# Optimization experiments

Hardware: AMD Instinct MI355X
Metric: run time of the kernel (lower is better)

Reference implementation:

```python
import jax, jax.numpy as jnp
import numpy as np


def setup_inputs() -> dict:
    key = jax.random.key(0)
    x = jax.random.normal(key, (4, 4096, 128), dtype=jnp.float32)
    return {"x": x}


def reference(x) -> jnp.ndarray:
    # Unnormalized bilinear self-attention with Q=K=V=x (no softmax).
    # scores[b,t,s] = sum_d x[b,t,d] x[b,s,d]; out[b,t,d] = sum_s scores[b,t,s] x[b,s,d]
    scores = jnp.einsum('btd,bsd->bts', x, x)  # [B,T,T]
    out = jnp.einsum('bts,bsd->btd', scores, x)  # [B,T,D]
    return out
```

## Files before the change

### kernel.cpp

```cpp
#include <hip/hip_runtime.h>

#define BATCH 4
#define T 4096
#define D 128
#define CHUNKS 64
#define ROWS1 64
#define ROWS2 64
#define ST1 72
#define S2 136

typedef __attribute__((ext_vector_type(4))) float f32x4;
typedef __attribute__((ext_vector_type(8))) short bf16x8;

__device__ __forceinline__ unsigned short f2b(float f) {
    unsigned u = __builtin_bit_cast(unsigned, f);
    u += 0x7FFFu + ((u >> 16) & 1u);
    return (unsigned short)(u >> 16);
}
__device__ __forceinline__ float b2f(unsigned short h) {
    return __builtin_bit_cast(float, (unsigned)h << 16);
}

__global__ __launch_bounds__(256) void k_gram(const float* __restrict__ x,
                                              unsigned short* __restrict__ part) {
    __shared__ unsigned short XT[D * ST1];
    const int blk = blockIdx.x;
    const int b = blk >> 6, chunk = blk & 63;
    const float* xp = x + ((size_t)b * T + (size_t)chunk * ROWS1) * D;
    const int tid = threadIdx.x;

    #pragma unroll
    for (int pass = 0; pass < 8; pass++) {
        const int slot = (tid >> 6) + 4 * pass;
        const int dd = 2 * (tid & 7) + 16 * (slot & 7);
        const int tpg = ((tid >> 3) & 7) + 8 * (slot >> 3);
        const int t = 2 * tpg;
        float2 f0 = *(const float2*)(xp + (size_t)t * D + dd);
        float2 f1 = *(const float2*)(xp + (size_t)(t + 1) * D + dd);
        unsigned u0 = (unsigned)f2b(f0.x) | ((unsigned)f2b(f1.x) << 16);
        unsigned u1 = (unsigned)f2b(f0.y) | ((unsigned)f2b(f1.y) << 16);
        *(unsigned*)(XT + dd * ST1 + 2 * tpg) = u0;
        *(unsigned*)(XT + (dd + 1) * ST1 + 2 * tpg) = u1;
    }
    __syncthreads();

    const int lane = tid & 63, w = tid >> 6;
    const int m = lane & 15, q = lane >> 4;
    const int m0 = w * 32;

    f32x4 acc[2][8];
    #pragma unroll
    for (int mi = 0; mi < 2; mi++)
        #pragma unroll
        for (int ni = 0; ni < 8; ni++) acc[mi][ni] = (f32x4){0.f, 0.f, 0.f, 0.f};

    #pragma unroll
    for (int s = 0; s < 2; s++) {
        bf16x8 av[2], bv[8];
        #pragma unroll
        for (int mi = 0; mi < 2; mi++)
            av[mi] = *(const bf16x8*)(XT + (m0 + mi * 16 + m) * ST1 + q * 8 + s * 32);
        #pragma unroll
        for (int ni = 0; ni < 8; ni++)
            bv[ni] = *(const bf16x8*)(XT + (ni * 16 + m) * ST1 + q * 8 + s * 32);
        #pragma unroll
        for (int mi = 0; mi < 2; mi++)
            #pragma unroll
            for (int ni = 0; ni < 8; ni++)
                acc[mi][ni] = __builtin_amdgcn_mfma_f32_16x16x32_bf16(av[mi], bv[ni], acc[mi][ni], 0, 0, 0);
    }

    unsigned short* pp = part + (size_t)blk * (D * D);
    #pragma unroll
    for (int mi = 0; mi < 2; mi++)
        #pragma unroll
        for (int ni = 0; ni < 8; ni++) {
            const int row0 = m0 + mi * 16 + q * 4;
            const int col = ni * 16 + m;
            #pragma unroll
            for (int r = 0; r < 4; r++)
                pp[(size_t)(row0 + r) * D + col] = f2b(acc[mi][ni][r]);
        }
}

__global__ __launch_bounds__(256) void k_reduce_g(const unsigned short* __restrict__ part,
                                                  unsigned short* __restrict__ g) {
    const int o = blockIdx.x * 256 + threadIdx.x;
    const int b = o >> 14;
    const int e = o & 16383;
    const unsigned short* p = part + ((size_t)b * CHUNKS) * (D * D) + e;
    float s[8];
    #pragma unroll
    for (int i = 0; i < 8; i++) s[i] = 0.f;
    for (int c = 0; c < CHUNKS; c += 8) {
        #pragma unroll
        for (int i = 0; i < 8; i++)
            s[i] += b2f(p[(size_t)(c + i) * (D * D)]);
    }
    float sum = ((s[0] + s[1]) + (s[2] + s[3])) + ((s[4] + s[5]) + (s[6] + s[7]));
    g[o] = f2b(sum);
}

__global__ __launch_bounds__(256) void k_xg_mfma(const float* __restrict__ x,
                                                 const unsigned short* __restrict__ g,
                                                 float* __restrict__ out) {
    __shared__ unsigned short Xs[ROWS2 * S2];
    __shared__ unsigned short Gs[D * S2];
    const int blk = blockIdx.x;
    const int b = blk >> 6, chunk = blk & 63;
    const float* xp = x + ((size_t)b * T + (size_t)chunk * ROWS2) * D;
    const unsigned short* gp = g + (size_t)b * (D * D);
    const int tid = threadIdx.x;

    {
        const int dg = tid & 31, tr = tid >> 5;
        #pragma unroll
        for (int ii = 0; ii < 8; ii++) {
            const int t = tr + ii * 8;
            float4 v = ((const float4*)(xp + t * D))[dg];
            ushort4 pk;
            pk.x = f2b(v.x); pk.y = f2b(v.y); pk.z = f2b(v.z); pk.w = f2b(v.w);
            *(ushort4*)(Xs + t * S2 + dg * 4) = pk;
        }
    }
    {
        const int f4 = tid & 15, r = tid >> 4;
        #pragma unroll
        for (int ii = 0; ii < 8; ii++) {
            const int row = r + ii * 16;
            uint4 gv = ((const uint4*)(gp + row * D))[f4];
            *(uint4*)(Gs + row * S2 + f4 * 8) = gv;
        }
    }
    __syncthreads();

    const int lane = tid & 63, w = tid >> 6;
    const int m = lane & 15, q = lane >> 4;

    f32x4 acc[8];
    #pragma unroll
    for (int ni = 0; ni < 8; ni++) acc[ni] = (f32x4){0.f, 0.f, 0.f, 0.f};

    const unsigned short* arow = Xs + (w * 16 + m) * S2 + q * 8;
    const unsigned short* brow = Gs + m * S2 + q * 8;

    #pragma unroll
    for (int s = 0; s < 4; s++) {
        bf16x8 a = *(const bf16x8*)(arow + s * 32);
        #pragma unroll
        for (int ni = 0; ni < 8; ni++) {
            bf16x8 bb = *(const bf16x8*)(brow + ni * 16 * S2 + s * 32);
            acc[ni] = __builtin_amdgcn_mfma_f32_16x16x32_bf16(a, bb, acc[ni], 0, 0, 0);
        }
    }

    float* op = out + ((size_t)b * T + (size_t)chunk * ROWS2) * D;
    const int row0 = w * 16 + q * 4;
    #pragma unroll
    for (int ni = 0; ni < 8; ni++)
        #pragma unroll
        for (int r = 0; r < 4; r++)
            op[(row0 + r) * D + ni * 16 + m] = acc[ni][r];
}

extern "C" void kernel_launch(void* const* d_in, const int* in_sizes, int n_in,
                              void* d_out, int out_size, void* d_ws, size_t ws_size,
                              hipStream_t stream) {
    const float* x = (const float*)d_in[0];
    float* out = (float*)d_out;

    const size_t part_elems = (size_t)BATCH * CHUNKS * D * D;
    unsigned short* part = (unsigned short*)d_ws;
    unsigned short* g = part + part_elems;

    k_gram<<<BATCH * CHUNKS, 256, 0, stream>>>(x, part);
    k_reduce_g<<<BATCH * D * D / 256, 256, 0, stream>>>(part, g);
    k_xg_mfma<<<BATCH * 64, 256, 0, stream>>>(x, g, out);
}
```

Before: 69.44 us.

## Fuse gram, reduce, and XG kernels into one cooperative kernel with grid syncs

Merges the three launches (per-chunk gram partials, cross-chunk reduction, X·G product) into one cooperative kernel that uses two grid-wide syncs in place of kernel boundaries. The bf16 row-major copy of X is kept in shared memory from the first phase, so the third phase does not reload and reconvert x from global memory. This removes two launch gaps and one pass over x, at the cost of grid-sync overhead and a requirement that all 256 blocks be co-resident.

```diff
diff --git a/kernel.cpp b/kernel.cpp
--- a/kernel.cpp
+++ b/kernel.cpp
@@ -1,11 +1,13 @@
 #include <hip/hip_runtime.h>
+#include <hip/hip_cooperative_groups.h>
+
+namespace cg = cooperative_groups;
 
 #define BATCH 4
 #define T 4096
 #define D 128
 #define CHUNKS 64
-#define ROWS1 64
-#define ROWS2 64
+#define ROWS 64
 #define ST1 72
 #define S2 136
 
@@ -21,14 +23,21 @@
     return __builtin_bit_cast(float, (unsigned)h << 16);
 }
 
-__global__ __launch_bounds__(256) void k_gram(const float* __restrict__ x,
-                                              unsigned short* __restrict__ part) {
-    __shared__ unsigned short XT[D * ST1];
+__global__ __launch_bounds__(256) void k_fused(const float* __restrict__ x,
+                                               unsigned short* __restrict__ part,
+                                               unsigned short* __restrict__ g,
+                                               float* __restrict__ out) {
+    __shared__ unsigned short Xs[ROWS * S2];
+    __shared__ unsigned short XG[D * S2];
+
     const int blk = blockIdx.x;
     const int b = blk >> 6, chunk = blk & 63;
-    const float* xp = x + ((size_t)b * T + (size_t)chunk * ROWS1) * D;
+    const float* xp = x + ((size_t)b * T + (size_t)chunk * ROWS) * D;
     const int tid = threadIdx.x;
+    const int lane = tid & 63, w = tid >> 6;
+    const int m = lane & 15, q = lane >> 4;
 
+    unsigned short* XT = XG;
     #pragma unroll
     for (int pass = 0; pass < 8; pass++) {
         const int slot = (tid >> 6) + 4 * pass;
@@ -37,93 +46,78 @@
         const int t = 2 * tpg;
         float2 f0 = *(const float2*)(xp + (size_t)t * D + dd);
         float2 f1 = *(const float2*)(xp + (size_t)(t + 1) * D + dd);
-        unsigned u0 = (unsigned)f2b(f0.x) | ((unsigned)f2b(f1.x) << 16);
-        unsigned u1 = (unsigned)f2b(f0.y) | ((unsigned)f2b(f1.y) << 16);
-        *(unsigned*)(XT + dd * ST1 + 2 * tpg) = u0;
-        *(unsigned*)(XT + (dd + 1) * ST1 + 2 * tpg) = u1;
+        const unsigned short b00 = f2b(f0.x), b01 = f2b(f0.y);
+        const unsigned short b10 = f2b(f1.x), b11 = f2b(f1.y);
+        *(unsigned*)(XT + dd * ST1 + 2 * tpg)       = (unsigned)b00 | ((unsigned)b10 << 16);
+        *(unsigned*)(XT + (dd + 1) * ST1 + 2 * tpg) = (unsigned)b01 | ((unsigned)b11 << 16);
+        *(unsigned*)(Xs + (size_t)t * S2 + dd)       = (unsigned)b00 | ((unsigned)b01 << 16);
+        *(unsigned*)(Xs + (size_t)(t + 1) * S2 + dd) = (unsigned)b10 | ((unsigned)b11 << 16);
     }
     __syncthreads();
 
-    const int lane = tid & 63, w = tid >> 6;
-    const int m = lane & 15, q = lane >> 4;
-    const int m0 = w * 32;
-
-    f32x4 acc[2][8];
-    #pragma unroll
-    for (int mi = 0; mi < 2; mi++)
-        #pragma unroll
-        for (int ni = 0; ni < 8; ni++) acc[mi][ni] = (f32x4){0.f, 0.f, 0.f, 0.f};
-
-    #pragma unroll
-    for (int s = 0; s < 2; s++) {
-        bf16x8 av[2], bv[8];
-        #pragma unroll
-        for (int mi = 0; mi < 2; mi++)
-            av[mi] = *(const bf16x8*)(XT + (m0 + mi * 16 + m) * ST1 + q * 8 + s * 32);
-        #pragma unroll
-        for (int ni = 0; ni < 8; ni++)
-            bv[ni] = *(const bf16x8*)(XT + (ni * 16 + m) * ST1 + q * 8 + s * 32);
+    {
+        const int m0 = w * 32;
+        f32x4 acc[2][8];
         #pragma unroll
         for (int mi = 0; mi < 2; mi++)
             #pragma unroll
+            for (int ni = 0; ni < 8; ni++) acc[mi][ni] = (f32x4){0.f, 0.f, 0.f, 0.f};
+
+        #pragma unroll
+        for (int s = 0; s < 2; s++) {
+            bf16x8 av[2], bv[8];
+            #pragma unroll
+            for (int mi = 0; mi < 2; mi++)
+                av[mi] = *(const bf16x8*)(XT + (m0 + mi * 16 + m) * ST1 + q * 8 + s * 32);
+            #pragma unroll
             for (int ni = 0; ni < 8; ni++)
-                acc[mi][ni] = __builtin_amdgcn_mfma_f32_16x16x32_bf16(av[mi], bv[ni], acc[mi][ni], 0, 0, 0);
+                bv[ni] = *(const bf16x8*)(XT + (ni * 16 + m) * ST1 + q * 8 + s * 32);
+            #pragma unroll
+            for (int mi = 0; mi < 2; mi++)
+                #pragma unroll
+                for (int ni = 0; ni < 8; ni++)
+                    acc[mi][ni] = __builtin_amdgcn_mfma_f32_16x16x32_bf16(av[mi], bv[ni], acc[mi][ni], 0, 0, 0);
+        }
+
+        unsigned short* pp = part + (size_t)blk * (D * D);
+        #pragma unroll
+        for (int mi = 0; mi < 2; mi++)
+            #pragma unroll
+            for (int ni = 0; ni < 8; ni++) {
+                const int row0 = m0 + mi * 16 + q * 4;
+                const int col = ni * 16 + m;
+                #pragma unroll
+                for (int r = 0; r < 4; r++)
+                    pp[(size_t)(row0 + r) * D + col] = f2b(acc[mi][ni][r]);
+            }
     }
 
-    unsigned short* pp = part + (size_t)blk * (D * D);
-    #pragma unroll
-    for (int mi = 0; mi < 2; mi++)
-        #pragma unroll
-        for (int ni = 0; ni < 8; ni++) {
-            const int row0 = m0 + mi * 16 + q * 4;
-            const int col = ni * 16 + m;
-            #pragma unroll
-            for (int r = 0; r < 4; r++)
-                pp[(size_t)(row0 + r) * D + col] = f2b(acc[mi][ni][r]);
-        }
-}
-
-__global__ __launch_bounds__(256) void k_reduce_g(const unsigned short* __restrict__ part,
-                                                  unsigned short* __restrict__ g) {
-    const int o = blockIdx.x * 256 + threadIdx.x;
-    const int b = o >> 14;
-    const int e = o & 16383;
-    const unsigned short* p = part + ((size_t)b * CHUNKS) * (D * D) + e;
-    float s[8];
-    #pragma unroll
-    for (int i = 0; i < 8; i++) s[i] = 0.f;
-    for (int c = 0; c < CHUNKS; c += 8) {
-        #pragma unroll
-        for (int i = 0; i < 8; i++)
-            s[i] += b2f(p[(size_t)(c + i) * (D * D)]);
-    }
-    float sum = ((s[0] + s[1]) + (s[2] + s[3])) + ((s[4] + s[5]) + (s[6] + s[7]));
-    g[o] = f2b(sum);
-}
-
-__global__ __launch_bounds__(256) void k_xg_mfma(const float* __restrict__ x,
-                                                 const unsigned short* __restrict__ g,
-                                                 float* __restrict__ out) {
-    __shared__ unsigned short Xs[ROWS2 * S2];
-    __shared__ unsigned short Gs[D * S2];
-    const int blk = blockIdx.x;
-    const int b = blk >> 6, chunk = blk & 63;
-    const float* xp = x + ((size_t)b * T + (size_t)chunk * ROWS2) * D;
-    const unsigned short* gp = g + (size_t)b * (D * D);
-    const int tid = threadIdx.x;
+    __threadfence();
+    cg::this_grid().sync();
 
     {
-        const int dg = tid & 31, tr = tid >> 5;
+        const int o = blk * 256 + tid;
+        const int bb = o >> 14;
+        const int e = o & 16383;
+        const unsigned short* p = part + ((size_t)bb * CHUNKS) * (D * D) + e;
+        float s[8];
         #pragma unroll
-        for (int ii = 0; ii < 8; ii++) {
-            const int t = tr + ii * 8;
-            float4 v = ((const float4*)(xp + t * D))[dg];
-            ushort4 pk;
-            pk.x = f2b(v.x); pk.y = f2b(v.y); pk.z = f2b(v.z); pk.w = f2b(v.w);
-            *(ushort4*)(Xs + t * S2 + dg * 4) = pk;
+        for (int i = 0; i < 8; i++) s[i] = 0.f;
+        for (int c = 0; c < CHUNKS; c += 8) {
+            #pragma unroll
+            for (int i = 0; i < 8; i++)
+                s[i] += b2f(p[(size_t)(c + i) * (D * D)]);
         }
+        float sum = ((s[0] + s[1]) + (s[2] + s[3])) + ((s[4] + s[5]) + (s[6] + s[7]));
+        g[o] = f2b(sum);
     }
+
+    __threadfence();
+    cg::this_grid().sync();
+
+    unsigned short* Gs = XG;
     {
+        const unsigned short* gp = g + (size_t)b * (D * D);
         const int f4 = tid & 15, r = tid >> 4;
         #pragma unroll
         for (int ii = 0; ii < 8; ii++) {
@@ -134,33 +128,32 @@
     }
     __syncthreads();
 
-    const int lane = tid & 63, w = tid >> 6;
-    const int m = lane & 15, q = lane >> 4;
+    {
+        f32x4 acc[8];
+        #pragma unroll
+        for (int ni = 0; ni < 8; ni++) acc[ni] = (f32x4){0.f, 0.f, 0.f, 0.f};
 
-    f32x4 acc[8];
-    #pragma unroll
-    for (int ni = 0; ni < 8; ni++) acc[ni] = (f32x4){0.f, 0.f, 0.f, 0.f};
+        const unsigned short* arow = Xs + (w * 16 + m) * S2 + q * 8;
+        const unsigned short* brow = Gs + m * S2 + q * 8;
 
-    const unsigned short* arow = Xs + (w * 16 + m) * S2 + q * 8;
-    const unsigned short* brow = Gs + m * S2 + q * 8;
+        #pragma unroll
+        for (int s = 0; s < 4; s++) {
+            bf16x8 a = *(const bf16x8*)(arow + s * 32);
+            #pragma unroll
+            for (int ni = 0; ni < 8; ni++) {
+                bf16x8 bb = *(const bf16x8*)(brow + ni * 16 * S2 + s * 32);
+                acc[ni] = __builtin_amdgcn_mfma_f32_16x16x32_bf16(a, bb, acc[ni], 0, 0, 0);
+            }
+        }
 
-    #pragma unroll
-    for (int s = 0; s < 4; s++) {
-        bf16x8 a = *(const bf16x8*)(arow + s * 32);
+        float* op = out + ((size_t)b * T + (size_t)chunk * ROWS) * D;
+        const int row0 = w * 16 + q * 4;
         #pragma unroll
-        for (int ni = 0; ni < 8; ni++) {
-            bf16x8 bb = *(const bf16x8*)(brow + ni * 16 * S2 + s * 32);
-            acc[ni] = __builtin_amdgcn_mfma_f32_16x16x32_bf16(a, bb, acc[ni], 0, 0, 0);
-        }
+        for (int ni = 0; ni < 8; ni++)
+            #pragma unroll
+            for (int r = 0; r < 4; r++)
+                op[(row0 + r) * D + ni * 16 + m] = acc[ni][r];
     }
-
-    float* op = out + ((size_t)b * T + (size_t)chunk * ROWS2) * D;
-    const int row0 = w * 16 + q * 4;
-    #pragma unroll
-    for (int ni = 0; ni < 8; ni++)
-        #pragma unroll
-        for (int r = 0; r < 4; r++)
-            op[(row0 + r) * D + ni * 16 + m] = acc[ni][r];
 }
 
 extern "C" void kernel_launch(void* const* d_in, const int* in_sizes, int n_in,
@@ -173,7 +166,7 @@
     unsigned short* part = (unsigned short*)d_ws;
     unsigned short* g = part + part_elems;
 
-    k_gram<<<BATCH * CHUNKS, 256, 0, stream>>>(x, part);
-    k_reduce_g<<<BATCH * D * D / 256, 256, 0, stream>>>(part, g);
-    k_xg_mfma<<<BATCH * 64, 256, 0, stream>>>(x, g, out);
+    void* args[4] = {(void*)&x, (void*)&part, (void*)&g, (void*)&out};
+    hipLaunchCooperativeKernel(reinterpret_cast<void*>(k_fused),
+                               dim3(BATCH * CHUNKS), dim3(256), args, 0, stream);
 }
```

Measured after the change: 191.4 us. 176% more time.

## Cut gram partials to 8 per batch and fold reduction into output kernel

Applied to the files above, without the earlier changes.

Each gram block now covers 512 rows, looping over 64-row sub-chunks with a double-buffered LDS stage, so only 8 partial 128x128 Gram matrices per batch are written instead of 64. The separate reduce kernel is removed: every output block re-sums the 8 partials for its batch into shared memory before the X·G MFMA. Block indices are remapped so blocks from different batches interleave. This drops a launch and most partial-matrix traffic, but the gram stage now runs only 32 blocks, which may leave most CUs idle, and every output block redundantly reads 8 partials.

```diff
diff --git a/kernel.cpp b/kernel.cpp
--- a/kernel.cpp
+++ b/kernel.cpp
@@ -3,9 +3,9 @@
 #define BATCH 4
 #define T 4096
 #define D 128
-#define CHUNKS 64
-#define ROWS1 64
-#define ROWS2 64
+#define P 8
+#define KROWS 512
+#define ROWS 64
 #define ST1 72
 #define S2 136
 
@@ -21,29 +21,30 @@
     return __builtin_bit_cast(float, (unsigned)h << 16);
 }
 
-__global__ __launch_bounds__(256) void k_gram(const float* __restrict__ x,
+#define STAGE_CHUNK(XPBASE, DST)                                               \
+    {                                                                          \
+        _Pragma("unroll")                                                      \
+        for (int pass = 0; pass < 8; pass++) {                                 \
+            const int slot = (tid >> 6) + 4 * pass;                            \
+            const int dd = 2 * (tid & 7) + 16 * (slot & 7);                    \
+            const int tpg = ((tid >> 3) & 7) + 8 * (slot >> 3);                \
+            const int t = 2 * tpg;                                             \
+            float2 f0 = *(const float2*)((XPBASE) + (size_t)t * D + dd);       \
+            float2 f1 = *(const float2*)((XPBASE) + (size_t)(t + 1) * D + dd); \
+            unsigned u0 = (unsigned)f2b(f0.x) | ((unsigned)f2b(f1.x) << 16);   \
+            unsigned u1 = (unsigned)f2b(f0.y) | ((unsigned)f2b(f1.y) << 16);   \
+            *(unsigned*)((DST) + dd * ST1 + 2 * tpg) = u0;                     \
+            *(unsigned*)((DST) + (dd + 1) * ST1 + 2 * tpg) = u1;               \
+        }                                                                      \
+    }
+
+__global__ __launch_bounds__(256) void k_part(const float* __restrict__ x,
                                               unsigned short* __restrict__ part) {
-    __shared__ unsigned short XT[D * ST1];
+    __shared__ unsigned short XT[2 * D * ST1];
     const int blk = blockIdx.x;
-    const int b = blk >> 6, chunk = blk & 63;
-    const float* xp = x + ((size_t)b * T + (size_t)chunk * ROWS1) * D;
+    const int b = blk >> 3, p = blk & 7;
+    const float* xp = x + ((size_t)b * T + (size_t)p * KROWS) * D;
     const int tid = threadIdx.x;
-
-    #pragma unroll
-    for (int pass = 0; pass < 8; pass++) {
-        const int slot = (tid >> 6) + 4 * pass;
-        const int dd = 2 * (tid & 7) + 16 * (slot & 7);
-        const int tpg = ((tid >> 3) & 7) + 8 * (slot >> 3);
-        const int t = 2 * tpg;
-        float2 f0 = *(const float2*)(xp + (size_t)t * D + dd);
-        float2 f1 = *(const float2*)(xp + (size_t)(t + 1) * D + dd);
-        unsigned u0 = (unsigned)f2b(f0.x) | ((unsigned)f2b(f1.x) << 16);
-        unsigned u1 = (unsigned)f2b(f0.y) | ((unsigned)f2b(f1.y) << 16);
-        *(unsigned*)(XT + dd * ST1 + 2 * tpg) = u0;
-        *(unsigned*)(XT + (dd + 1) * ST1 + 2 * tpg) = u1;
-    }
-    __syncthreads();
-
     const int lane = tid & 63, w = tid >> 6;
     const int m = lane & 15, q = lane >> 4;
     const int m0 = w * 32;
@@ -54,20 +55,33 @@
         #pragma unroll
         for (int ni = 0; ni < 8; ni++) acc[mi][ni] = (f32x4){0.f, 0.f, 0.f, 0.f};
 
+    STAGE_CHUNK(xp, XT);
+    __syncthreads();
+
     #pragma unroll
-    for (int s = 0; s < 2; s++) {
-        bf16x8 av[2], bv[8];
+    for (int i = 0; i < 8; i++) {
+        const unsigned short* cur = XT + (i & 1) * (D * ST1);
+        if (i < 7) {
+            unsigned short* nxt = XT + ((i + 1) & 1) * (D * ST1);
+            const float* xn = xp + (size_t)(i + 1) * ROWS * D;
+            STAGE_CHUNK(xn, nxt);
+        }
         #pragma unroll
-        for (int mi = 0; mi < 2; mi++)
-            av[mi] = *(const bf16x8*)(XT + (m0 + mi * 16 + m) * ST1 + q * 8 + s * 32);
-        #pragma unroll
-        for (int ni = 0; ni < 8; ni++)
-            bv[ni] = *(const bf16x8*)(XT + (ni * 16 + m) * ST1 + q * 8 + s * 32);
-        #pragma unroll
-        for (int mi = 0; mi < 2; mi++)
+        for (int s = 0; s < 2; s++) {
+            bf16x8 av[2], bv[8];
+            #pragma unroll
+            for (int mi = 0; mi < 2; mi++)
+                av[mi] = *(const bf16x8*)(cur + (m0 + mi * 16 + m) * ST1 + q * 8 + s * 32);
             #pragma unroll
             for (int ni = 0; ni < 8; ni++)
-                acc[mi][ni] = __builtin_amdgcn_mfma_f32_16x16x32_bf16(av[mi], bv[ni], acc[mi][ni], 0, 0, 0);
+                bv[ni] = *(const bf16x8*)(cur + (ni * 16 + m) * ST1 + q * 8 + s * 32);
+            #pragma unroll
+            for (int mi = 0; mi < 2; mi++)
+                #pragma unroll
+                for (int ni = 0; ni < 8; ni++)
+                    acc[mi][ni] = __builtin_amdgcn_mfma_f32_16x16x32_bf16(av[mi], bv[ni], acc[mi][ni], 0, 0, 0);
+        }
+        __syncthreads();
     }
 
     unsigned short* pp = part + (size_t)blk * (D * D);
@@ -83,33 +97,15 @@
         }
 }
 
-__global__ __launch_bounds__(256) void k_reduce_g(const unsigned short* __restrict__ part,
-                                                  unsigned short* __restrict__ g) {
-    const int o = blockIdx.x * 256 + threadIdx.x;
-    const int b = o >> 14;
-    const int e = o & 16383;
-    const unsigned short* p = part + ((size_t)b * CHUNKS) * (D * D) + e;
-    float s[8];
-    #pragma unroll
-    for (int i = 0; i < 8; i++) s[i] = 0.f;
-    for (int c = 0; c < CHUNKS; c += 8) {
-        #pragma unroll
-        for (int i = 0; i < 8; i++)
-            s[i] += b2f(p[(size_t)(c + i) * (D * D)]);
-    }
-    float sum = ((s[0] + s[1]) + (s[2] + s[3])) + ((s[4] + s[5]) + (s[6] + s[7]));
-    g[o] = f2b(sum);
-}
-
-__global__ __launch_bounds__(256) void k_xg_mfma(const float* __restrict__ x,
-                                                 const unsigned short* __restrict__ g,
-                                                 float* __restrict__ out) {
-    __shared__ unsigned short Xs[ROWS2 * S2];
+__global__ __launch_bounds__(256) void k_xg2(const float* __restrict__ x,
+                                             const unsigned short* __restrict__ part,
+                                             float* __restrict__ out) {
+    __shared__ unsigned short Xs[ROWS * S2];
     __shared__ unsigned short Gs[D * S2];
     const int blk = blockIdx.x;
-    const int b = blk >> 6, chunk = blk & 63;
-    const float* xp = x + ((size_t)b * T + (size_t)chunk * ROWS2) * D;
-    const unsigned short* gp = g + (size_t)b * (D * D);
+    const int b = (blk & 7) >> 1;
+    const int chunk = ((blk & 1) << 5) | (blk >> 3);
+    const float* xp = x + ((size_t)b * T + (size_t)chunk * ROWS) * D;
     const int tid = threadIdx.x;
 
     {
@@ -117,50 +113,69 @@
         #pragma unroll
         for (int ii = 0; ii < 8; ii++) {
             const int t = tr + ii * 8;
-            float4 v = ((const float4*)(xp + t * D))[dg];
+            float4 v = ((const float4*)(xp + (size_t)t * D))[dg];
             ushort4 pk;
             pk.x = f2b(v.x); pk.y = f2b(v.y); pk.z = f2b(v.z); pk.w = f2b(v.w);
             *(ushort4*)(Xs + t * S2 + dg * 4) = pk;
         }
     }
     {
-        const int f4 = tid & 15, r = tid >> 4;
+        const unsigned short* pb = part + (size_t)b * P * (D * D);
         #pragma unroll
-        for (int ii = 0; ii < 8; ii++) {
-            const int row = r + ii * 16;
-            uint4 gv = ((const uint4*)(gp + row * D))[f4];
-            *(uint4*)(Gs + row * S2 + f4 * 8) = gv;
+        for (int i = 0; i < 8; i++) {
+            const int e8 = (i * 256 + tid) * 8;
+            float s[8];
+            #pragma unroll
+            for (int k = 0; k < 8; k++) s[k] = 0.f;
+            #pragma unroll
+            for (int pp = 0; pp < P; pp++) {
+                uint4 v = *(const uint4*)(pb + (size_t)pp * (D * D) + e8);
+                const unsigned uu[4] = {v.x, v.y, v.z, v.w};
+                #pragma unroll
+                for (int k = 0; k < 4; k++) {
+                    s[2 * k]     += __builtin_bit_cast(float, uu[k] << 16);
+                    s[2 * k + 1] += __builtin_bit_cast(float, uu[k] & 0xFFFF0000u);
+                }
+            }
+            uint4 o;
+            o.x = (unsigned)f2b(s[0]) | ((unsigned)f2b(s[1]) << 16);
+            o.y = (unsigned)f2b(s[2]) | ((unsigned)f2b(s[3]) << 16);
+            o.z = (unsigned)f2b(s[4]) | ((unsigned)f2b(s[5]) << 16);
+            o.w = (unsigned)f2b(s[6]) | ((unsigned)f2b(s[7]) << 16);
+            const int row = e8 >> 7, col = e8 & 127;
+            *(uint4*)(Gs + row * S2 + col) = o;
         }
     }
     __syncthreads();
 
-    const int lane = tid & 63, w = tid >> 6;
-    const int m = lane & 15, q = lane >> 4;
+    {
+        const int lane = tid & 63, w = tid >> 6;
+        const int m = lane & 15, q = lane >> 4;
+        f32x4 acc[8];
+        #pragma unroll
+        for (int ni = 0; ni < 8; ni++) acc[ni] = (f32x4){0.f, 0.f, 0.f, 0.f};
 
-    f32x4 acc[8];
-    #pragma unroll
-    for (int ni = 0; ni < 8; ni++) acc[ni] = (f32x4){0.f, 0.f, 0.f, 0.f};
+        const unsigned short* arow = Xs + (w * 16 + m) * S2 + q * 8;
+        const unsigned short* brow = Gs + m * S2 + q * 8;
 
-    const unsigned short* arow = Xs + (w * 16 + m) * S2 + q * 8;
-    const unsigned short* brow = Gs + m * S2 + q * 8;
+        #pragma unroll
+        for (int s = 0; s < 4; s++) {
+            bf16x8 a = *(const bf16x8*)(arow + s * 32);
+            #pragma unroll
+            for (int ni = 0; ni < 8; ni++) {
+                bf16x8 bb = *(const bf16x8*)(brow + ni * 16 * S2 + s * 32);
+                acc[ni] = __builtin_amdgcn_mfma_f32_16x16x32_bf16(a, bb, acc[ni], 0, 0, 0);
+            }
+        }
 
-    #pragma unroll
-    for (int s = 0; s < 4; s++) {
-        bf16x8 a = *(const bf16x8*)(arow + s * 32);
+        float* op = out + ((size_t)b * T + (size_t)chunk * ROWS) * D;
+        const int row0 = w * 16 + q * 4;
         #pragma unroll
-        for (int ni = 0; ni < 8; ni++) {
-            bf16x8 bb = *(const bf16x8*)(brow + ni * 16 * S2 + s * 32);
-            acc[ni] = __builtin_amdgcn_mfma_f32_16x16x32_bf16(a, bb, acc[ni], 0, 0, 0);
-        }
+        for (int ni = 0; ni < 8; ni++)
+            #pragma unroll
+            for (int r = 0; r < 4; r++)
+                op[(row0 + r) * D + ni * 16 + m] = acc[ni][r];
     }
-
-    float* op = out + ((size_t)b * T + (size_t)chunk * ROWS2) * D;
-    const int row0 = w * 16 + q * 4;
-    #pragma unroll
-    for (int ni = 0; ni < 8; ni++)
-        #pragma unroll
-        for (int r = 0; r < 4; r++)
-            op[(row0 + r) * D + ni * 16 + m] = acc[ni][r];
 }
 
 extern "C" void kernel_launch(void* const* d_in, const int* in_sizes, int n_in,
@@ -169,11 +184,8 @@
     const float* x = (const float*)d_in[0];
     float* out = (float*)d_out;
 
-    const size_t part_elems = (size_t)BATCH * CHUNKS * D * D;
     unsigned short* part = (unsigned short*)d_ws;
-    unsigned short* g = part + part_elems;
 
-    k_gram<<<BATCH * CHUNKS, 256, 0, stream>>>(x, part);
-    k_reduce_g<<<BATCH * D * D / 256, 256, 0, stream>>>(part, g);
-    k_xg_mfma<<<BATCH * 64, 256, 0, stream>>>(x, g, out);
+    k_part<<<BATCH * P, 256, 0, stream>>>(x, part);
+    k_xg2<<<BATCH * 64, 256, 0, stream>>>(x, part, out);
 }
```

Result: slower. 88.64 us (+27.7%).
